# Performance work log

Hardware: AMD Instinct MI355X
Metric: run time of the kernel (lower is better)

The kernel has to match this reference:

```python
import jax, jax.numpy as jnp
import numpy as np

EPS = 1e-12  # torch F.normalize eps


def setup_inputs() -> dict:
    key = jax.random.key(0)
    k1, k2, k3 = jax.random.split(key, 3)
    B, D, H, W, K = 64, 512, 32, 32, 64
    x = jax.random.normal(k1, (B, D, H, W), dtype=jnp.float32)
    w = jax.random.normal(k2, (K, D), dtype=jnp.float32) * 0.05  # 1x1 conv weight
    c = jax.random.normal(k3, (K, D), dtype=jnp.float32)          # cluster centers
    return {"x": x, "w": w, "c": c}


def reference(x, w, c):
    B, D, H, W = x.shape
    K = w.shape[0]
    N = H * W
    # 1x1 conv (no bias): (B,D,H,W) x (K,D) -> (B,K,H,W)
    features = jnp.einsum('bdhw,kd->bkhw', x, w)
    # NOTE: original applies softmax over dim=2 (the H axis only)
    a_bar = jax.nn.softmax(features, axis=2)
    xf = x.reshape(B, D, N)
    a = a_bar.reshape(B, K, N)
    # V[b,k,d] = sum_n a[b,k,n] * (x[b,d,n] - c[k,d])
    V = jnp.einsum('bkn,bdn->bkd', a, xf) - a.sum(axis=2)[:, :, None] * c[None]
    V = V.transpose(2, 1, 0)  # (D, K, B)
    # F.normalize(V, p=2, dim=1) applied twice (second is idempotent)
    norm = jnp.maximum(jnp.linalg.norm(V, axis=1, keepdims=True), EPS)
    y = V / norm
    norm2 = jnp.maximum(jnp.linalg.norm(y, axis=1, keepdims=True), EPS)
    return y / norm2
```

## Files before the change

### kernel.cpp

```cpp
#include <hip/hip_runtime.h>


typedef __attribute__((ext_vector_type(8))) short short8;
typedef __attribute__((ext_vector_type(4))) float f32x4;
typedef unsigned short u16;
typedef unsigned int u32;

union S8u { u32 q[4]; short8 s; };

__device__ __forceinline__ u32 pk2(float lo, float hi) {
  union { float f; u32 u; } a, b; a.f = lo; b.f = hi;
  u32 xl = (a.u + 0x7fffu + ((a.u >> 16) & 1u)) >> 16;
  u32 xh = (b.u + 0x7fffu + ((b.u >> 16) & 1u)) & 0xffff0000u;
  return xl | xh;
}

__device__ __forceinline__ u16 bf1(float f) {
  union { float f; u32 u; } a; a.f = f;
  return (u16)((a.u + 0x7fffu + ((a.u >> 16) & 1u)) >> 16);
}

typedef const __attribute__((address_space(1))) u32 GU32;
typedef __attribute__((address_space(3))) u32 LU32;
__device__ __forceinline__ void glds16(const void* g, void* l) {
  __builtin_amdgcn_global_load_lds((GU32*)g, (LU32*)l, 16, 0, 0);
}

__global__ __launch_bounds__(256) void k0_packw(
    const float* __restrict__ w, u16* __restrict__ wsw)
{
  const int tg = blockIdx.x * 256 + threadIdx.x;
  const int dd4 = tg & 7, i = (tg >> 3) & 15, k = tg >> 7;
  f32x4 v = *(const f32x4*)(w + k * 512 + i * 32 + dd4 * 4);
  u32* dst = (u32*)(wsw + ((size_t)i * 64 + k) * 40 + dd4 * 4);
  dst[0] = pk2(v[0], v[1]);
  dst[1] = pk2(v[2], v[3]);
}

__global__ __launch_bounds__(256, 2) void k1_features(
    const float* __restrict__ x, const u16* __restrict__ wsw,
    float* __restrict__ feat)
{
  const int blk = blockIdx.x;
  const int b = blk & 63, nt8 = blk >> 6;
  const int nb = nt8 * 128;
  const int tid = threadIdx.x, lane = tid & 63, wv = tid >> 6;
  const int row = lane & 15, q = lane >> 4;

  __shared__ __align__(16) float xs[2][32][128];
  __shared__ __align__(16) u16 wls[2][64][40];

  const char* xbase = (const char*)(x + ((size_t)b << 19) + nb);
  const char* wbase = (const char*)wsw;
  const int dd0 = tid >> 5, cby = (tid & 31) * 16;

  f32x4 acc[4][2];
#pragma unroll
  for (int mt = 0; mt < 4; mt++)
#pragma unroll
    for (int nt = 0; nt < 2; nt++) acc[mt][nt] = (f32x4){0.f, 0.f, 0.f, 0.f};

#define STAGE1(d0, buf)                                                        \
  {                                                                            \
    char* lx = (char*)&xs[buf][0][0];                                          \
    _Pragma("unroll")                                                          \
    for (int j = 0; j < 4; j++) {                                              \
      const int dd = j * 8 + dd0;                                              \
      glds16(xbase + (size_t)((d0) + dd) * 4096 + cby,                         \
             lx + j * 4096 + tid * 16);                                        \
    }                                                                          \
    char* lw = (char*)&wls[buf][0][0];                                         \
    const char* gw = wbase + (size_t)((d0) >> 5) * 5120;                       \
    glds16(gw + tid * 16, lw + tid * 16);                                      \
    if (tid < 64) glds16(gw + 4096 + tid * 16, lw + 4096 + tid * 16);          \
  }

  STAGE1(0, 0);
  for (int i = 0; i < 16; i++) {
    const int buf = i & 1;
    __syncthreads();
    if (i < 15) STAGE1((i + 1) * 32, buf ^ 1);

    short8 af[4];
#pragma unroll
    for (int mt = 0; mt < 4; mt++)
      af[mt] = *(const short8*)&wls[buf][mt * 16 + row][q * 8];
    short8 bfv[2];
#pragma unroll
    for (int nt = 0; nt < 2; nt++) {
      const int n = wv * 32 + nt * 16 + row;
      const int d8 = q * 8;
      float v0 = xs[buf][d8 + 0][n], v1 = xs[buf][d8 + 1][n];
      float v2 = xs[buf][d8 + 2][n], v3 = xs[buf][d8 + 3][n];
      float v4 = xs[buf][d8 + 4][n], v5 = xs[buf][d8 + 5][n];
      float v6 = xs[buf][d8 + 6][n], v7 = xs[buf][d8 + 7][n];
      S8u t;
      t.q[0] = pk2(v0, v1); t.q[1] = pk2(v2, v3);
      t.q[2] = pk2(v4, v5); t.q[3] = pk2(v6, v7);
      bfv[nt] = t.s;
    }
#pragma unroll
    for (int nt = 0; nt < 2; nt++)
#pragma unroll
      for (int mt = 0; mt < 4; mt++)
        acc[mt][nt] = __builtin_amdgcn_mfma_f32_16x16x32_bf16(af[mt], bfv[nt], acc[mt][nt], 0, 0, 0);
  }
#undef STAGE1

  float* fb = feat + ((size_t)b << 16);
  const int nbw = nb + wv * 32;
#pragma unroll
  for (int mt = 0; mt < 4; mt++)
#pragma unroll
    for (int nt = 0; nt < 2; nt++)
#pragma unroll
      for (int r = 0; r < 4; r++)
        fb[(mt * 16 + q * 4 + r) * 1024 + nbw + nt * 16 + row] = acc[mt][nt][r];
}

__global__ __launch_bounds__(256) void k1b_softmax(
    const float* __restrict__ feat, u16* __restrict__ apad)
{
  const int tid = threadIdx.x, lane = tid & 63, wv = tid >> 6;
  const int rid = blockIdx.x * 4 + wv;
  const int b = rid >> 6, k = rid & 63;
  const float* f = feat + ((size_t)rid << 10);
  const int w = lane & 31, half = lane >> 5;
  const int base = w + half * 512;
  float v[16];
  float m = -1e30f;
#pragma unroll
  for (int i = 0; i < 16; i++) { v[i] = f[base + i * 32]; m = fmaxf(m, v[i]); }
  m = fmaxf(m, __shfl_xor(m, 32));
  float s = 0.f;
#pragma unroll
  for (int i = 0; i < 16; i++) { v[i] = __expf(v[i] - m); s += v[i]; }
  s += __shfl_xor(s, 32);
  const float inv = 1.0f / s;
#pragma unroll
  for (int i = 0; i < 16; i++) {
    const int h = half * 16 + i;
    apad[((size_t)(b * 32 + h) * 64 + k) * 40 + w] = bf1(v[i] * inv);
  }
}

__global__ __launch_bounds__(256, 2) void k2_aggregate(
    const float* __restrict__ x, const u16* __restrict__ apad,
    const float* __restrict__ cc, float* __restrict__ yw)
{
  const int blk = blockIdx.x;
  const int b = blk & 63, dt = blk >> 6;
  const int tid = threadIdx.x, lane = tid & 63, wv = tid >> 6;
  const int row = lane & 15, q = lane >> 4;

  __shared__ __align__(16) u16 als[2][64][40];

  const char* abase = (const char*)(apad + (size_t)b * 32 * 64 * 40);
  const float* px0 = x + ((size_t)b << 19) + (size_t)(dt * 64 + wv * 16 + row) * 1024 + q * 8;

#define STAGEA(i, buf)                                                         \
  {                                                                            \
    char* la = (char*)&als[buf][0][0];                                         \
    const char* ga = abase + (size_t)(i) * 5120;                               \
    glds16(ga + tid * 16, la + tid * 16);                                      \
    if (tid < 64) glds16(ga + 4096 + tid * 16, la + 4096 + tid * 16);          \
  }

  f32x4 acc[4];
#pragma unroll
  for (int mt = 0; mt < 4; mt++) acc[mt] = (f32x4){0.f, 0.f, 0.f, 0.f};

  STAGEA(0, 0);
  f32x4 c0 = *(const f32x4*)px0;
  f32x4 c1 = *(const f32x4*)(px0 + 4);
  f32x4 p0, p1;
  for (int i = 0; i < 32; i++) {
    const int buf = i & 1;
    __syncthreads();
    if (i < 31) {
      STAGEA(i + 1, buf ^ 1);
      p0 = *(const f32x4*)(px0 + (i + 1) * 32);
      p1 = *(const f32x4*)(px0 + (i + 1) * 32 + 4);
    }
    S8u t;
    t.q[0] = pk2(c0[0], c0[1]); t.q[1] = pk2(c0[2], c0[3]);
    t.q[2] = pk2(c1[0], c1[1]); t.q[3] = pk2(c1[2], c1[3]);
    const short8 bfv = t.s;
#pragma unroll
    for (int mt = 0; mt < 4; mt++) {
      short8 af = *(const short8*)&als[buf][mt * 16 + row][q * 8];
      acc[mt] = __builtin_amdgcn_mfma_f32_16x16x32_bf16(af, bfv, acc[mt], 0, 0, 0);
    }
    c0 = p0; c1 = p1;
  }
#undef STAGEA

  const int dcol = dt * 64 + wv * 16 + row;
  float v[16]; float ss = 0.f;
#pragma unroll
  for (int mt = 0; mt < 4; mt++)
#pragma unroll
    for (int r = 0; r < 4; r++) {
      const int k = mt * 16 + q * 4 + r;
      const float tv = acc[mt][r] - 32.0f * cc[k * 512 + dcol];
      v[mt * 4 + r] = tv; ss += tv * tv;
    }
  ss += __shfl_xor(ss, 16);
  ss += __shfl_xor(ss, 32);
  const float rn = 1.0f / fmaxf(sqrtf(ss), 1e-12f);
  float* yb = yw + ((size_t)b << 15) + dcol;
#pragma unroll
  for (int mt = 0; mt < 4; mt++)
#pragma unroll
    for (int r = 0; r < 4; r++)
      yb[(size_t)(mt * 16 + q * 4 + r) << 9] = v[mt * 4 + r] * rn;
}

__global__ __launch_bounds__(256) void k3_transpose(
    const float* __restrict__ yw, float* __restrict__ out)
{
  const int blk = blockIdx.x;
  const int k = blk & 63;
  const int dt = blk >> 6;
  const int d0 = dt * 64;
  const int tid = threadIdx.x;
  __shared__ float T[64][68];
  {
    const int bl = tid >> 2, seg = tid & 3;
    const float* src = yw + (size_t)bl * 32768 + k * 512 + d0 + seg * 16;
#pragma unroll
    for (int i = 0; i < 4; i++) {
      f32x4 v = *(const f32x4*)(src + i * 4);
#pragma unroll
      for (int jj = 0; jj < 4; jj++) T[seg * 16 + i * 4 + jj][bl] = v[jj];
    }
  }
  __syncthreads();
  {
    const int dl = tid >> 2, bseg = tid & 3;
    float* dst = out + (size_t)(d0 + dl) * 4096 + k * 64 + bseg * 16;
    const float* srcT = &T[dl][bseg * 16];
#pragma unroll
    for (int i = 0; i < 4; i++)
      *(f32x4*)(dst + i * 4) = *(const f32x4*)(srcT + i * 4);
  }
}

extern "C" void kernel_launch(void* const* d_in, const int* in_sizes, int n_in,
                              void* d_out, int out_size, void* d_ws, size_t ws_size,
                              hipStream_t stream) {
  const float* x = (const float*)d_in[0];
  const float* w = (const float*)d_in[1];
  const float* c = (const float*)d_in[2];
  float* out = (float*)d_out;
  char* ws = (char*)d_ws;
  float* feat = (float*)ws;
  u16*   apad = (u16*)(ws + (size_t)16 * 1024 * 1024);
  float* yw   = (float*)(ws + (size_t)26 * 1024 * 1024);
  u16*   wsw  = (u16*)(ws + (size_t)34 * 1024 * 1024);
  k0_packw    <<<dim3(32),   dim3(256), 0, stream>>>(w, wsw);
  k1_features <<<dim3(512),  dim3(256), 0, stream>>>(x, wsw, feat);
  k1b_softmax <<<dim3(1024), dim3(256), 0, stream>>>(feat, apad);
  k2_aggregate<<<dim3(512),  dim3(256), 0, stream>>>(x, apad, c, yw);
  k3_transpose<<<dim3(512),  dim3(256), 0, stream>>>(yw, out);
}
```

Measured before the change: 231.9 us.

## Triple-buffer LDS staging with vmcnt waits and vectorize softmax stores

Both the feature GEMM and the aggregate kernel switch from double to triple-buffered global-to-LDS staging. They prefetch two stages ahead and replace __syncthreads with explicit vmcnt waits plus raw barriers, so loads stay in flight across iterations. The softmax kernel is reorganized so each lane handles 4 contiguous w values with float4 loads and packed bf16 pair stores, instead of scalar strided accesses. The cost is more LDS per block, which may reduce occupancy, and correctness now depends on hand-counted vmcnt values matching the number of outstanding loads.

Measured after the change: 235.1 us. Within noise of the previous version (+1.4%).

```diff
diff --git a/kernel.cpp b/kernel.cpp
--- a/kernel.cpp
+++ b/kernel.cpp
@@ -13,11 +13,6 @@
   u32 xl = (a.u + 0x7fffu + ((a.u >> 16) & 1u)) >> 16;
   u32 xh = (b.u + 0x7fffu + ((b.u >> 16) & 1u)) & 0xffff0000u;
   return xl | xh;
-}
-
-__device__ __forceinline__ u16 bf1(float f) {
-  union { float f; u32 u; } a; a.f = f;
-  return (u16)((a.u + 0x7fffu + ((a.u >> 16) & 1u)) >> 16);
 }
 
 typedef const __attribute__((address_space(1))) u32 GU32;
@@ -47,8 +42,8 @@
   const int tid = threadIdx.x, lane = tid & 63, wv = tid >> 6;
   const int row = lane & 15, q = lane >> 4;
 
-  __shared__ __align__(16) float xs[2][32][128];
-  __shared__ __align__(16) u16 wls[2][64][40];
+  __shared__ __align__(16) float xs[3][32][128];
+  __shared__ __align__(16) u16 wls[3][64][40];
 
   const char* xbase = (const char*)(x + ((size_t)b << 19) + nb);
   const char* wbase = (const char*)wsw;
@@ -76,24 +71,31 @@
   }
 
   STAGE1(0, 0);
+  STAGE1(32, 1);
+  int bi = 0;
   for (int i = 0; i < 16; i++) {
-    const int buf = i & 1;
-    __syncthreads();
-    if (i < 15) STAGE1((i + 1) * 32, buf ^ 1);
+    if (i == 15) asm volatile("s_waitcnt vmcnt(0)" ::: "memory");
+    else         asm volatile("s_waitcnt vmcnt(5)" ::: "memory");
+    __builtin_amdgcn_s_barrier();
+    __builtin_amdgcn_sched_barrier(0);
+    if (i < 14) {
+      const int nbuf = (bi == 0) ? 2 : bi - 1;
+      STAGE1((i + 2) * 32, nbuf);
+    }
 
     short8 af[4];
 #pragma unroll
     for (int mt = 0; mt < 4; mt++)
-      af[mt] = *(const short8*)&wls[buf][mt * 16 + row][q * 8];
+      af[mt] = *(const short8*)&wls[bi][mt * 16 + row][q * 8];
     short8 bfv[2];
 #pragma unroll
     for (int nt = 0; nt < 2; nt++) {
       const int n = wv * 32 + nt * 16 + row;
       const int d8 = q * 8;
-      float v0 = xs[buf][d8 + 0][n], v1 = xs[buf][d8 + 1][n];
-      float v2 = xs[buf][d8 + 2][n], v3 = xs[buf][d8 + 3][n];
-      float v4 = xs[buf][d8 + 4][n], v5 = xs[buf][d8 + 5][n];
-      float v6 = xs[buf][d8 + 6][n], v7 = xs[buf][d8 + 7][n];
+      float v0 = xs[bi][d8 + 0][n], v1 = xs[bi][d8 + 1][n];
+      float v2 = xs[bi][d8 + 2][n], v3 = xs[bi][d8 + 3][n];
+      float v4 = xs[bi][d8 + 4][n], v5 = xs[bi][d8 + 5][n];
+      float v6 = xs[bi][d8 + 6][n], v7 = xs[bi][d8 + 7][n];
       S8u t;
       t.q[0] = pk2(v0, v1); t.q[1] = pk2(v2, v3);
       t.q[2] = pk2(v4, v5); t.q[3] = pk2(v6, v7);
@@ -104,6 +106,8 @@
 #pragma unroll
       for (int mt = 0; mt < 4; mt++)
         acc[mt][nt] = __builtin_amdgcn_mfma_f32_16x16x32_bf16(af[mt], bfv[nt], acc[mt][nt], 0, 0, 0);
+
+    bi = (bi == 2) ? 0 : bi + 1;
   }
 #undef STAGE1
 
@@ -121,26 +125,48 @@
 __global__ __launch_bounds__(256) void k1b_softmax(
     const float* __restrict__ feat, u16* __restrict__ apad)
 {
-  const int tid = threadIdx.x, lane = tid & 63, wv = tid >> 6;
+  const int tid = threadIdx.x, wv = tid >> 6, lane = tid & 63;
   const int rid = blockIdx.x * 4 + wv;
   const int b = rid >> 6, k = rid & 63;
   const float* f = feat + ((size_t)rid << 10);
-  const int w = lane & 31, half = lane >> 5;
-  const int base = w + half * 512;
-  float v[16];
-  float m = -1e30f;
-#pragma unroll
-  for (int i = 0; i < 16; i++) { v[i] = f[base + i * 32]; m = fmaxf(m, v[i]); }
-  m = fmaxf(m, __shfl_xor(m, 32));
-  float s = 0.f;
-#pragma unroll
-  for (int i = 0; i < 16; i++) { v[i] = __expf(v[i] - m); s += v[i]; }
-  s += __shfl_xor(s, 32);
-  const float inv = 1.0f / s;
-#pragma unroll
-  for (int i = 0; i < 16; i++) {
-    const int h = half * 16 + i;
-    apad[((size_t)(b * 32 + h) * 64 + k) * 40 + w] = bf1(v[i] * inv);
+  const int wl = (lane & 7) * 4;
+  const int hq = lane >> 3;
+
+  f32x4 v[4];
+#pragma unroll
+  for (int r = 0; r < 4; r++)
+    v[r] = *(const f32x4*)(f + (hq + r * 8) * 32 + wl);
+
+  f32x4 m = v[0];
+#pragma unroll
+  for (int r = 1; r < 4; r++)
+#pragma unroll
+    for (int c = 0; c < 4; c++) m[c] = fmaxf(m[c], v[r][c]);
+#pragma unroll
+  for (int mk = 8; mk <= 32; mk <<= 1)
+#pragma unroll
+    for (int c = 0; c < 4; c++) m[c] = fmaxf(m[c], __shfl_xor(m[c], mk));
+
+  f32x4 s = (f32x4){0.f, 0.f, 0.f, 0.f};
+#pragma unroll
+  for (int r = 0; r < 4; r++)
+#pragma unroll
+    for (int c = 0; c < 4; c++) { v[r][c] = __expf(v[r][c] - m[c]); s[c] += v[r][c]; }
+#pragma unroll
+  for (int mk = 8; mk <= 32; mk <<= 1)
+#pragma unroll
+    for (int c = 0; c < 4; c++) s[c] += __shfl_xor(s[c], mk);
+
+  f32x4 inv;
+#pragma unroll
+  for (int c = 0; c < 4; c++) inv[c] = 1.0f / s[c];
+
+#pragma unroll
+  for (int r = 0; r < 4; r++) {
+    const int h = hq + r * 8;
+    u32* dst = (u32*)(apad + ((size_t)(b * 32 + h) * 64 + k) * 40 + wl);
+    dst[0] = pk2(v[r][0] * inv[0], v[r][1] * inv[1]);
+    dst[1] = pk2(v[r][2] * inv[2], v[r][3] * inv[3]);
   }
 }
 
@@ -153,7 +179,7 @@
   const int tid = threadIdx.x, lane = tid & 63, wv = tid >> 6;
   const int row = lane & 15, q = lane >> 4;
 
-  __shared__ __align__(16) u16 als[2][64][40];
+  __shared__ __align__(16) u16 als[3][64][40];
 
   const char* abase = (const char*)(apad + (size_t)b * 32 * 64 * 40);
   const float* px0 = x + ((size_t)b << 19) + (size_t)(dt * 64 + wv * 16 + row) * 1024 + q * 8;
@@ -173,14 +199,21 @@
   STAGEA(0, 0);
   f32x4 c0 = *(const f32x4*)px0;
   f32x4 c1 = *(const f32x4*)(px0 + 4);
-  f32x4 p0, p1;
+  STAGEA(1, 1);
+  int bi = 0;
   for (int i = 0; i < 32; i++) {
-    const int buf = i & 1;
-    __syncthreads();
+    if (i == 31) asm volatile("s_waitcnt vmcnt(0)" ::: "memory");
+    else         asm volatile("s_waitcnt vmcnt(3)" ::: "memory");
+    __builtin_amdgcn_s_barrier();
+    __builtin_amdgcn_sched_barrier(0);
+    f32x4 p0, p1;
     if (i < 31) {
-      STAGEA(i + 1, buf ^ 1);
       p0 = *(const f32x4*)(px0 + (i + 1) * 32);
       p1 = *(const f32x4*)(px0 + (i + 1) * 32 + 4);
+    }
+    if (i < 30) {
+      const int nbuf = (bi == 0) ? 2 : bi - 1;
+      STAGEA(i + 2, nbuf);
     }
     S8u t;
     t.q[0] = pk2(c0[0], c0[1]); t.q[1] = pk2(c0[2], c0[3]);
@@ -188,10 +221,11 @@
     const short8 bfv = t.s;
 #pragma unroll
     for (int mt = 0; mt < 4; mt++) {
-      short8 af = *(const short8*)&als[buf][mt * 16 + row][q * 8];
+      short8 af = *(const short8*)&als[bi][mt * 16 + row][q * 8];
       acc[mt] = __builtin_amdgcn_mfma_f32_16x16x32_bf16(af, bfv, acc[mt], 0, 0, 0);
     }
     c0 = p0; c1 = p1;
+    bi = (bi == 2) ? 0 : bi + 1;
   }
 #undef STAGEA
 
```
